# Performance work log

Hardware: AMD Instinct MI355X
Metric: run time of the kernel (lower is better)

## Reference

```python
import jax, jax.numpy as jnp
import numpy as np

B, T, N, F_IN, F_OUT, K = 4, 32, 1024, 128, 128, 4


def setup_inputs() -> dict:
    key = jax.random.key(0)
    k1, k2, k3 = jax.random.split(key, 3)
    X = jax.random.normal(k1, (B, T, N, F_IN), dtype=jnp.float32)
    # graph-shift operator; 1/sqrt(N) scaling keeps S^k products numerically tame
    S = jax.random.normal(k2, (N, N), dtype=jnp.float32) / np.float32(np.sqrt(N))
    W = jax.random.normal(k3, (F_OUT, F_IN, K), dtype=jnp.float32) * 0.1
    b = jnp.zeros((F_OUT,), dtype=jnp.float32)
    return {"X": X, "S": S, "W": W, "b": b}


def reference(X, S, W, b):
    # Y[:, t] = sum_{k=0}^{K-1, t-k>=0} S^k @ X[:, t-k] @ W[:, :, k]^T + b
    # (static graph: the per-(t,k) shift-chain product in the original collapses to S^k)
    Bsz, Tlen, Nn, Fin = X.shape
    Kord = W.shape[-1]
    Y = jnp.zeros((Bsz, Tlen, Nn, W.shape[0]), X.dtype)
    Z = X  # Z = S^k @ X, starting at k=0 (identity)
    for k in range(Kord):
        # causal time-shift by k: output at t uses Z at t-k (zeros for t-k<0)
        Zs = Z if k == 0 else jnp.pad(Z, ((0, 0), (k, 0), (0, 0), (0, 0)))[:, :Tlen]
        Y = Y + jnp.einsum('btnf,of->btno', Zs, W[:, :, k])
        if k < Kord - 1:
            Z = jnp.einsum('nm,btmf->btnf', S, Z)  # advance shift power
    return Y + b
```

## Files before the change

kernel.cpp:

```cpp
#include <hip/hip_runtime.h>
#include <stdint.h>

#define BT 128
#define NN 1024
#define FF 128

typedef __attribute__((ext_vector_type(8))) short short8;
typedef __attribute__((ext_vector_type(4))) float float4v;
typedef __attribute__((ext_vector_type(4))) unsigned short ushort4v;

__device__ __forceinline__ unsigned short f2bf(float f) {
  uint32_t u = __builtin_bit_cast(uint32_t, f);
  u += 0x7FFFu + ((u >> 16) & 1u);
  return (unsigned short)(u >> 16);
}

__device__ __forceinline__ void gload16(const void* g, void* l) {
  __builtin_amdgcn_global_load_lds(
      (const __attribute__((address_space(1))) uint32_t*)(g),
      (__attribute__((address_space(3))) uint32_t*)(l),
      16, 0, 0);
}

__global__ __launch_bounds__(256) void k_cvt_sw(const float* __restrict__ S,
                                                unsigned short* __restrict__ Sbf,
                                                unsigned short* __restrict__ SbfT,
                                                const float* __restrict__ W,
                                                unsigned short* __restrict__ Wk2) {
  __shared__ unsigned short tile[128 * 132];
  int tid = threadIdx.x;
  if (blockIdx.x >= 64) {
    int gid = (blockIdx.x - 64) * 256 + tid;
    int k = gid >> 14, o = (gid >> 7) & 127, f = gid & 127;
    Wk2[gid] = f2bf(W[(o * 128 + f) * 4 + k]);
    return;
  }
  int r0 = ((int)blockIdx.x >> 3) << 7;
  int c0 = ((int)blockIdx.x & 7) << 7;
#pragma unroll
  for (int i = 0; i < 16; ++i) {
    int idx = i * 256 + tid;
    int r = idx >> 5, cq = idx & 31;
    float4v v = reinterpret_cast<const float4v*>(S)[(size_t)(r0 + r) * 256 + (c0 >> 2) + cq];
    ushort4v h;
    h[0] = f2bf(v[0]); h[1] = f2bf(v[1]); h[2] = f2bf(v[2]); h[3] = f2bf(v[3]);
    *reinterpret_cast<ushort4v*>(&Sbf[(size_t)(r0 + r) * 1024 + c0 + cq * 4]) = h;
    *reinterpret_cast<ushort4v*>(&tile[r * 132 + cq * 4]) = h;
  }
  __syncthreads();
#pragma unroll
  for (int i = 0; i < 16; ++i) {
    int idx = i * 256 + tid;
    int c = idx >> 5, rq = idx & 31;
    ushort4v h;
#pragma unroll
    for (int j = 0; j < 4; ++j) h[j] = tile[(rq * 4 + j) * 132 + c];
    *reinterpret_cast<ushort4v*>(&SbfT[(size_t)(c0 + c) * 1024 + r0 + rq * 4]) = h;
  }
}

__global__ __launch_bounds__(256) void k_cvt_x(const float* __restrict__ X,
                                               unsigned short* __restrict__ Xbf,
                                               unsigned short* __restrict__ Xt) {
  __shared__ unsigned short tile[128 * 132];
  int bt = blockIdx.x >> 3;
  int n0 = (blockIdx.x & 7) << 7;
  int tid = threadIdx.x;
  size_t base = ((size_t)bt * NN + n0) * FF;
#pragma unroll
  for (int i = 0; i < 16; ++i) {
    int idx = i * 256 + tid;
    int e = idx * 4;
    int n = e >> 7, f = e & 127;
    float4v v = reinterpret_cast<const float4v*>(X + base)[idx];
    ushort4v h;
    h[0] = f2bf(v[0]); h[1] = f2bf(v[1]); h[2] = f2bf(v[2]); h[3] = f2bf(v[3]);
    reinterpret_cast<ushort4v*>(Xbf + base)[idx] = h;
    *reinterpret_cast<ushort4v*>(&tile[n * 132 + f]) = h;
  }
  __syncthreads();
  size_t tbase = (size_t)bt * (FF * NN);
#pragma unroll
  for (int i = 0; i < 64; ++i) {
    int idx = i * 256 + tid;
    int f = idx >> 7, n = idx & 127;
    Xt[tbase + (size_t)f * NN + n0 + n] = tile[n * 132 + f];
  }
}

__global__ __launch_bounds__(256) void gemm_s(const unsigned short* __restrict__ A,
                                              const unsigned short* __restrict__ B,
                                              unsigned short* __restrict__ C) {
  __shared__ unsigned short lA[128 * 64];
  __shared__ unsigned short lB[128 * 64];
  int r0 = ((int)blockIdx.x >> 3) << 7;
  int c0 = ((int)blockIdx.x & 7) << 7;
  int tid = threadIdx.x;
  int wave = tid >> 6, lane = tid & 63;
  int wr = wave >> 1, wc = wave & 1;
  int lr = lane & 15, g = lane >> 4;

  const unsigned short* gA = A + (size_t)r0 * 1024;
  const unsigned short* gB = B + (size_t)c0 * 1024;

  float4v acc[4][4];
#pragma unroll
  for (int a = 0; a < 4; ++a)
#pragma unroll
    for (int b = 0; b < 4; ++b) acc[a][b] = (float4v){0.f, 0.f, 0.f, 0.f};

  for (int kt = 0; kt < 16; ++kt) {
    int m0 = kt * 64;
#pragma unroll
    for (int i = 0; i < 4; ++i) {
      int id = i * 256 + tid;
      int row = id >> 3;
      int mc = (id & 7) << 3;
      int slot = (i * 256 + (tid & 192)) * 8;
      gload16(gA + (size_t)row * 1024 + m0 + mc, &lA[slot]);
      gload16(gB + (size_t)row * 1024 + m0 + mc, &lB[slot]);
    }
    __syncthreads();
#pragma unroll
    for (int kk = 0; kk < 2; ++kk) {
      short8 aF[4], bF[4];
#pragma unroll
      for (int mi = 0; mi < 4; ++mi)
        aF[mi] = *reinterpret_cast<const short8*>(
            &lA[(wr * 64 + mi * 16 + lr) * 64 + kk * 32 + g * 8]);
#pragma unroll
      for (int ni = 0; ni < 4; ++ni)
        bF[ni] = *reinterpret_cast<const short8*>(
            &lB[(wc * 64 + ni * 16 + lr) * 64 + kk * 32 + g * 8]);
#pragma unroll
      for (int mi = 0; mi < 4; ++mi)
#pragma unroll
        for (int ni = 0; ni < 4; ++ni)
          acc[mi][ni] = __builtin_amdgcn_mfma_f32_16x16x32_bf16(
              aF[mi], bF[ni], acc[mi][ni], 0, 0, 0);
    }
    __syncthreads();
  }

#pragma unroll
  for (int mi = 0; mi < 4; ++mi) {
#pragma unroll
    for (int ni = 0; ni < 4; ++ni) {
      int rr = r0 + wr * 64 + mi * 16 + g * 4;
      int cc = c0 + wc * 64 + ni * 16 + lr;
#pragma unroll
      for (int j = 0; j < 4; ++j)
        C[(size_t)(rr + j) * 1024 + cc] = f2bf(acc[mi][ni][j]);
    }
  }
}

__global__ __launch_bounds__(512, 2) void k_chain8(
    const unsigned short* __restrict__ Xt,
    const unsigned short* __restrict__ S1,
    const unsigned short* __restrict__ S2,
    const unsigned short* __restrict__ S3,
    unsigned short* __restrict__ Zn1,
    unsigned short* __restrict__ Zn2,
    unsigned short* __restrict__ Zn3) {
  extern __shared__ unsigned char lds[];

  int bid = blockIdx.x;
  int logical = (bid & 7) * 96 + (bid >> 3);
  int cblk = logical / 12;
  int pkn = logical - cblk * 12;
  int power = pkn >> 2, nblk = pkn & 3;
  const unsigned short* Sp = (power == 0) ? S1 : ((power == 1) ? S2 : S3);
  unsigned short* Zn = (power == 0) ? Zn1 : ((power == 1) ? Zn2 : Zn3);

  int tid = threadIdx.x;
  int wave = tid >> 6, lane = tid & 63;
  int wave_m = wave >> 2, wave_n = wave & 3;
  int lr = lane & 15, g = lane >> 4;

  unsigned srcO[4][2], dstO[4][2];
#pragma unroll
  for (int j = 0; j < 2; ++j) {
    int sr0 = wave * 16 + j * 8;
    int rbA = (sr0 & 63) + ((sr0 >> 6) << 7);
    int rbB = (sr0 & 31) + ((sr0 >> 5) << 6);
    int seg = lane & 7;
    int rA0 = rbA + (lane >> 3), rA1 = rA0 + 64;
    int rB0 = rbB + (lane >> 3), rB1 = rB0 + 32;
    srcO[0][j] = (unsigned)(cblk * 256 + rA0) * 1024u + (unsigned)((seg ^ (rA0 & 7)) << 3);
    srcO[3][j] = (unsigned)(cblk * 256 + rA1) * 1024u + (unsigned)((seg ^ (rA1 & 7)) << 3);
    srcO[1][j] = (unsigned)(nblk * 256 + rB0) * 1024u + (unsigned)((seg ^ (rB0 & 7)) << 3);
    srcO[2][j] = (unsigned)(nblk * 256 + rB1) * 1024u + (unsigned)((seg ^ (rB1 & 7)) << 3);
    dstO[0][j] = (unsigned)rbA * 128u;
    dstO[3][j] = (unsigned)(rbA + 64) * 128u;
    dstO[1][j] = 32768u + (unsigned)rbB * 128u;
    dstO[2][j] = 32768u + (unsigned)(rbB + 32) * 128u;
  }

  const unsigned xm = (unsigned)((lr & 7) << 4);
  const unsigned xo0 = ((unsigned)(g * 16)) ^ xm;
  const unsigned xo1 = ((unsigned)(64 + g * 16)) ^ xm;
  const unsigned aRB = (unsigned)((wave_m * 128 + lr) * 128);
  const unsigned bRB = 32768u + (unsigned)((wave_n * 64 + lr) * 128);

#define RD(OFF) (*reinterpret_cast<const short8*>(lds + (OFF)))

  float4v acc[8][4];
#pragma unroll
  for (int a = 0; a < 8; ++a)
#pragma unroll
    for (int b = 0; b < 4; ++b) acc[a][b] = (float4v){0.f, 0.f, 0.f, 0.f};

  short8 aF[4][2], bF[2][2], cF[2][2];

#pragma unroll
  for (int j = 0; j < 2; ++j) gload16(Xt + srcO[0][j], lds + dstO[0][j]);
#pragma unroll
  for (int j = 0; j < 2; ++j) gload16(Sp + srcO[1][j], lds + dstO[1][j]);
#pragma unroll
  for (int j = 0; j < 2; ++j) gload16(Sp + srcO[2][j], lds + dstO[2][j]);
#pragma unroll
  for (int j = 0; j < 2; ++j) gload16(Xt + srcO[3][j], lds + dstO[3][j]);
  asm volatile("s_waitcnt vmcnt(0)" ::: "memory");
  __builtin_amdgcn_s_barrier();

  for (int kt = 0; kt < 16; ++kt) {
    const unsigned bo = (unsigned)(kt & 1) << 16;
    const unsigned nbo = bo ^ 65536u;
    const unsigned ko = (unsigned)(kt + 1) * 64u;
    const bool st = (kt < 15);

#pragma unroll
    for (int mf = 0; mf < 4; ++mf) {
      aF[mf][0] = RD(bo + aRB + (unsigned)mf * 2048u + xo0);
      aF[mf][1] = RD(bo + aRB + (unsigned)mf * 2048u + xo1);
    }
#pragma unroll
    for (int nf = 0; nf < 2; ++nf) {
      bF[nf][0] = RD(bo + bRB + (unsigned)nf * 2048u + xo0);
      bF[nf][1] = RD(bo + bRB + (unsigned)nf * 2048u + xo1);
    }
    if (st) {
      gload16(Xt + srcO[0][0] + ko, lds + nbo + dstO[0][0]);
      gload16(Xt + srcO[0][1] + ko, lds + nbo + dstO[0][1]);
      asm volatile("s_waitcnt lgkmcnt(8) vmcnt(4)" ::: "memory");
    } else {
      asm volatile("s_waitcnt lgkmcnt(8) vmcnt(2)" ::: "memory");
    }
    __builtin_amdgcn_s_barrier();
    asm volatile("s_waitcnt lgkmcnt(0)" ::: "memory");
    __builtin_amdgcn_sched_barrier(0);
    __builtin_amdgcn_s_setprio(1);
#pragma unroll
    for (int mf = 0; mf < 4; ++mf)
#pragma unroll
      for (int nf = 0; nf < 2; ++nf) {
        acc[mf][nf] = __builtin_amdgcn_mfma_f32_16x16x32_bf16(aF[mf][0], bF[nf][0], acc[mf][nf], 0, 0, 0);
        acc[mf][nf] = __builtin_amdgcn_mfma_f32_16x16x32_bf16(aF[mf][1], bF[nf][1], acc[mf][nf], 0, 0, 0);
      }
    __builtin_amdgcn_s_setprio(0);
    __builtin_amdgcn_sched_barrier(0);
    __builtin_amdgcn_s_barrier();
    __builtin_amdgcn_sched_barrier(0);

#pragma unroll
    for (int nf = 0; nf < 2; ++nf) {
      cF[nf][0] = RD(bo + bRB + 4096u + (unsigned)nf * 2048u + xo0);
      cF[nf][1] = RD(bo + bRB + 4096u + (unsigned)nf * 2048u + xo1);
    }
    if (st) {
      gload16(Sp + srcO[1][0] + ko, lds + nbo + dstO[1][0]);
      gload16(Sp + srcO[1][1] + ko, lds + nbo + dstO[1][1]);
      asm volatile("s_waitcnt vmcnt(4)" ::: "memory");
    } else {
      asm volatile("s_waitcnt vmcnt(0)" ::: "memory");
    }
    __builtin_amdgcn_s_barrier();
    asm volatile("s_waitcnt lgkmcnt(0)" ::: "memory");
    __builtin_amdgcn_sched_barrier(0);
    __builtin_amdgcn_s_setprio(1);
#pragma unroll
    for (int mf = 0; mf < 4; ++mf)
#pragma unroll
      for (int nf = 0; nf < 2; ++nf) {
        acc[mf][2 + nf] = __builtin_amdgcn_mfma_f32_16x16x32_bf16(aF[mf][0], cF[nf][0], acc[mf][2 + nf], 0, 0, 0);
        acc[mf][2 + nf] = __builtin_amdgcn_mfma_f32_16x16x32_bf16(aF[mf][1], cF[nf][1], acc[mf][2 + nf], 0, 0, 0);
      }
    __builtin_amdgcn_s_setprio(0);
    __builtin_amdgcn_sched_barrier(0);
    __builtin_amdgcn_s_barrier();
    __builtin_amdgcn_sched_barrier(0);

#pragma unroll
    for (int mf = 0; mf < 4; ++mf) {
      aF[mf][0] = RD(bo + aRB + 8192u + (unsigned)mf * 2048u + xo0);
      aF[mf][1] = RD(bo + aRB + 8192u + (unsigned)mf * 2048u + xo1);
    }
    if (st) {
      gload16(Sp + srcO[2][0] + ko, lds + nbo + dstO[2][0]);
      gload16(Sp + srcO[2][1] + ko, lds + nbo + dstO[2][1]);
    }
    __builtin_amdgcn_s_barrier();
    asm volatile("s_waitcnt lgkmcnt(0)" ::: "memory");
    __builtin_amdgcn_sched_barrier(0);
    __builtin_amdgcn_s_setprio(1);
#pragma unroll
    for (int mf = 0; mf < 4; ++mf)
#pragma unroll
      for (int nf = 0; nf < 2; ++nf) {
        acc[4 + mf][nf] = __builtin_amdgcn_mfma_f32_16x16x32_bf16(aF[mf][0], bF[nf][0], acc[4 + mf][nf], 0, 0, 0);
        acc[4 + mf][nf] = __builtin_amdgcn_mfma_f32_16x16x32_bf16(aF[mf][1], bF[nf][1], acc[4 + mf][nf], 0, 0, 0);
      }
    __builtin_amdgcn_s_setprio(0);
    __builtin_amdgcn_sched_barrier(0);
    __builtin_amdgcn_s_barrier();
    __builtin_amdgcn_sched_barrier(0);

    if (st) {
      gload16(Xt + srcO[3][0] + ko, lds + nbo + dstO[3][0]);
      gload16(Xt + srcO[3][1] + ko, lds + nbo + dstO[3][1]);
      asm volatile("s_waitcnt vmcnt(4)" ::: "memory");
    }
    __builtin_amdgcn_s_barrier();
    __builtin_amdgcn_sched_barrier(0);
    __builtin_amdgcn_s_setprio(1);
#pragma unroll
    for (int mf = 0; mf < 4; ++mf)
#pragma unroll
      for (int nf = 0; nf < 2; ++nf) {
        acc[4 + mf][2 + nf] = __builtin_amdgcn_mfma_f32_16x16x32_bf16(aF[mf][0], cF[nf][0], acc[4 + mf][2 + nf], 0, 0, 0);
        acc[4 + mf][2 + nf] = __builtin_amdgcn_mfma_f32_16x16x32_bf16(aF[mf][1], cF[nf][1], acc[4 + mf][2 + nf], 0, 0, 0);
      }
    __builtin_amdgcn_s_setprio(0);
    __builtin_amdgcn_sched_barrier(0);
    __builtin_amdgcn_s_barrier();
    __builtin_amdgcn_sched_barrier(0);
  }
#undef RD

  int bt = cblk * 2 + wave_m;
  size_t zbase = (size_t)bt * (NN * FF);
  int nb = nblk * 256 + wave_n * 64 + lr;
#pragma unroll
  for (int i = 0; i < 8; ++i) {
#pragma unroll
    for (int j2 = 0; j2 < 4; ++j2) {
      int n = nb + j2 * 16;
      int f0 = i * 16 + g * 4;
      ushort4v pk;
#pragma unroll
      for (int j = 0; j < 4; ++j) pk[j] = f2bf(acc[i][j2][j]);
      *reinterpret_cast<ushort4v*>(&Zn[zbase + (size_t)n * FF + f0]) = pk;
    }
  }
}

__global__ __launch_bounds__(256) void k_out(const unsigned short* __restrict__ Xbf,
                                             const unsigned short* __restrict__ Zn1,
                                             const unsigned short* __restrict__ Zn2,
                                             const unsigned short* __restrict__ Zn3,
                                             const unsigned short* __restrict__ Wk2,
                                             const float* __restrict__ bias,
                                             float* __restrict__ Y) {
  __shared__ unsigned short lA[128 * 64];
  __shared__ unsigned short lB[128 * 64];
  int bid = blockIdx.x;
  int bt = bid >> 3;
  int n0 = (bid & 7) << 7;
  int t = bt & 31;
  int tid = threadIdx.x;
  int wave = tid >> 6, lane = tid & 63;
  int wr = wave >> 1, wc = wave & 1;
  int lr = lane & 15, g = lane >> 4;

  const unsigned short* Zs[4] = {Xbf, Zn1, Zn2, Zn3};

  float4v acc[4][4];
#pragma unroll
  for (int a = 0; a < 4; ++a)
#pragma unroll
    for (int b = 0; b < 4; ++b) acc[a][b] = (float4v){0.f, 0.f, 0.f, 0.f};

  for (int s = 0; s < 8; ++s) {
    int k = s >> 1;
    if (t < k) break;
    int fh = (s & 1) * 64;
    const unsigned short* gA = Zs[k] + ((size_t)(bt - k) * NN + n0) * FF;
    const unsigned short* gB = Wk2 + k * (FF * FF);
#pragma unroll
    for (int i = 0; i < 4; ++i) {
      int id = i * 256 + tid;
      int row = id >> 3;
      int fc = (id & 7) << 3;
      int slot = (i * 256 + (tid & 192)) * 8;
      gload16(gA + (size_t)row * FF + fh + fc, &lA[slot]);
      gload16(gB + (size_t)row * FF + fh + fc, &lB[slot]);
    }
    __syncthreads();
#pragma unroll
    for (int kk = 0; kk < 2; ++kk) {
      short8 aF[4], bF[4];
#pragma unroll
      for (int mi = 0; mi < 4; ++mi)
        aF[mi] = *reinterpret_cast<const short8*>(
            &lA[(wr * 64 + mi * 16 + lr) * 64 + kk * 32 + g * 8]);
#pragma unroll
      for (int ni = 0; ni < 4; ++ni)
        bF[ni] = *reinterpret_cast<const short8*>(
            &lB[(wc * 64 + ni * 16 + lr) * 64 + kk * 32 + g * 8]);
#pragma unroll
      for (int mi = 0; mi < 4; ++mi)
#pragma unroll
        for (int ni = 0; ni < 4; ++ni)
          acc[mi][ni] = __builtin_amdgcn_mfma_f32_16x16x32_bf16(
              aF[mi], bF[ni], acc[mi][ni], 0, 0, 0);
    }
    __syncthreads();
  }

  size_t obase = (size_t)bt * (NN * FF);
#pragma unroll
  for (int mi = 0; mi < 4; ++mi) {
#pragma unroll
    for (int ni = 0; ni < 4; ++ni) {
      int nloc = n0 + wr * 64 + mi * 16 + g * 4;
      int o = wc * 64 + ni * 16 + lr;
      float bv = bias[o];
#pragma unroll
      for (int j = 0; j < 4; ++j)
        Y[obase + (size_t)(nloc + j) * FF + o] = acc[mi][ni][j] + bv;
    }
  }
}


extern "C" void kernel_launch(void* const* d_in, const int* in_sizes, int n_in,
                              void* d_out, int out_size, void* d_ws, size_t ws_size,
                              hipStream_t stream) {
  const float* X = (const float*)d_in[0];
  const float* S = (const float*)d_in[1];
  const float* W = (const float*)d_in[2];
  const float* bvec = (const float*)d_in[3];
  float* Y = (float*)d_out;

  char* ws = (char*)d_ws;
  const size_t ZB = (size_t)BT * NN * FF * sizeof(unsigned short);
  const size_t SB = (size_t)1024 * 1024 * sizeof(unsigned short);
  unsigned short* Xt   = (unsigned short*)(ws + 0 * ZB);
  unsigned short* Zn1  = (unsigned short*)(ws + 1 * ZB);
  unsigned short* Zn2  = (unsigned short*)(ws + 2 * ZB);
  unsigned short* Zn3  = (unsigned short*)(ws + 3 * ZB);
  unsigned short* Xbf  = (unsigned short*)(ws + 4 * ZB);
  unsigned short* Sbf  = (unsigned short*)(ws + 5 * ZB);
  unsigned short* SbfT = (unsigned short*)(ws + 5 * ZB + 1 * SB);
  unsigned short* S2   = (unsigned short*)(ws + 5 * ZB + 2 * SB);
  unsigned short* S3   = (unsigned short*)(ws + 5 * ZB + 3 * SB);
  unsigned short* Wk2  = (unsigned short*)(ws + 5 * ZB + 4 * SB);

  k_cvt_sw<<<dim3(320), dim3(256), 0, stream>>>(S, Sbf, SbfT, W, Wk2);
  k_cvt_x<<<dim3(1024), dim3(256), 0, stream>>>(X, Xbf, Xt);

  gemm_s<<<dim3(64), dim3(256), 0, stream>>>(Sbf, SbfT, S2);
  gemm_s<<<dim3(64), dim3(256), 0, stream>>>(S2, SbfT, S3);

  hipError_t _e = hipFuncSetAttribute((const void*)k_chain8,
                      hipFuncAttributeMaxDynamicSharedMemorySize, 131072);
  (void)_e;
  k_chain8<<<dim3(768), dim3(512), 131072, stream>>>(Xt, Sbf, S2, S3, Zn1, Zn2, Zn3);

  k_out<<<dim3(1024), dim3(256), 0, stream>>>(Xbf, Zn1, Zn2, Zn3, Wk2, bvec, Y);
}
```

Baseline: 220.2 us.

## Restructure filter as Horner recurrence with fused time-shift and weight projection

Replaces the S^2/S^3 precompute, the three-power chain GEMM and the separate output GEMM with a Horner-style recurrence. It projects X by W3 first, then runs three S-multiply stages, each adding a fresh X·Wk projection in its epilogue, with the time shift done by reading the previous timestep (or a zero buffer). This drops the 1024^3 S-power GEMMs, the transposes and the 4-term output pass, cutting total work. In exchange it needs three dependent chain launches with only 256 blocks each, and error may compound through repeated bf16 rounding of the intermediates.

```diff
diff --git a/kernel.cpp b/kernel.cpp
--- a/kernel.cpp
+++ b/kernel.cpp
@@ -24,84 +24,59 @@
 
 __global__ __launch_bounds__(256) void k_cvt_sw(const float* __restrict__ S,
                                                 unsigned short* __restrict__ Sbf,
-                                                unsigned short* __restrict__ SbfT,
                                                 const float* __restrict__ W,
-                                                unsigned short* __restrict__ Wk2) {
-  __shared__ unsigned short tile[128 * 132];
+                                                unsigned short* __restrict__ Wk2,
+                                                unsigned short* __restrict__ zbuf) {
   int tid = threadIdx.x;
-  if (blockIdx.x >= 64) {
-    int gid = (blockIdx.x - 64) * 256 + tid;
+  int b = blockIdx.x;
+  if (b < 64) {
+#pragma unroll
+    for (int i = 0; i < 16; ++i) {
+      int g4 = b * 4096 + i * 256 + tid;
+      float4v v = reinterpret_cast<const float4v*>(S)[g4];
+      ushort4v h;
+      h[0] = f2bf(v[0]); h[1] = f2bf(v[1]); h[2] = f2bf(v[2]); h[3] = f2bf(v[3]);
+      reinterpret_cast<ushort4v*>(Sbf)[g4] = h;
+    }
+  } else if (b < 320) {
+    int gid = (b - 64) * 256 + tid;
     int k = gid >> 14, o = (gid >> 7) & 127, f = gid & 127;
     Wk2[gid] = f2bf(W[(o * 128 + f) * 4 + k]);
-    return;
-  }
-  int r0 = ((int)blockIdx.x >> 3) << 7;
-  int c0 = ((int)blockIdx.x & 7) << 7;
-#pragma unroll
-  for (int i = 0; i < 16; ++i) {
-    int idx = i * 256 + tid;
-    int r = idx >> 5, cq = idx & 31;
-    float4v v = reinterpret_cast<const float4v*>(S)[(size_t)(r0 + r) * 256 + (c0 >> 2) + cq];
+  } else {
+    ushort4v z = (ushort4v){0, 0, 0, 0};
+#pragma unroll
+    for (int i = 0; i < 16; ++i)
+      reinterpret_cast<ushort4v*>(zbuf)[(b - 320) * 4096 + i * 256 + tid] = z;
+  }
+}
+
+__global__ __launch_bounds__(256) void k_cvt_x(const float* __restrict__ X,
+                                               unsigned short* __restrict__ Xbf) {
+  int base = blockIdx.x * 1024 + threadIdx.x;
+#pragma unroll
+  for (int i = 0; i < 4; ++i) {
+    int g4 = base + i * 256;
+    float4v v = reinterpret_cast<const float4v*>(X)[g4];
     ushort4v h;
     h[0] = f2bf(v[0]); h[1] = f2bf(v[1]); h[2] = f2bf(v[2]); h[3] = f2bf(v[3]);
-    *reinterpret_cast<ushort4v*>(&Sbf[(size_t)(r0 + r) * 1024 + c0 + cq * 4]) = h;
-    *reinterpret_cast<ushort4v*>(&tile[r * 132 + cq * 4]) = h;
-  }
-  __syncthreads();
-#pragma unroll
-  for (int i = 0; i < 16; ++i) {
-    int idx = i * 256 + tid;
-    int c = idx >> 5, rq = idx & 31;
-    ushort4v h;
-#pragma unroll
-    for (int j = 0; j < 4; ++j) h[j] = tile[(rq * 4 + j) * 132 + c];
-    *reinterpret_cast<ushort4v*>(&SbfT[(size_t)(c0 + c) * 1024 + r0 + rq * 4]) = h;
-  }
-}
-
-__global__ __launch_bounds__(256) void k_cvt_x(const float* __restrict__ X,
-                                               unsigned short* __restrict__ Xbf,
-                                               unsigned short* __restrict__ Xt) {
-  __shared__ unsigned short tile[128 * 132];
+    reinterpret_cast<ushort4v*>(Xbf)[g4] = h;
+  }
+}
+
+__global__ __launch_bounds__(256) void k_proj(const unsigned short* __restrict__ Wk2,
+                                              const unsigned short* __restrict__ Xbf,
+                                              unsigned short* __restrict__ U3) {
+  __shared__ unsigned short lA[128 * 64];
+  __shared__ unsigned short lB[128 * 64];
   int bt = blockIdx.x >> 3;
   int n0 = (blockIdx.x & 7) << 7;
-  int tid = threadIdx.x;
-  size_t base = ((size_t)bt * NN + n0) * FF;
-#pragma unroll
-  for (int i = 0; i < 16; ++i) {
-    int idx = i * 256 + tid;
-    int e = idx * 4;
-    int n = e >> 7, f = e & 127;
-    float4v v = reinterpret_cast<const float4v*>(X + base)[idx];
-    ushort4v h;
-    h[0] = f2bf(v[0]); h[1] = f2bf(v[1]); h[2] = f2bf(v[2]); h[3] = f2bf(v[3]);
-    reinterpret_cast<ushort4v*>(Xbf + base)[idx] = h;
-    *reinterpret_cast<ushort4v*>(&tile[n * 132 + f]) = h;
-  }
-  __syncthreads();
-  size_t tbase = (size_t)bt * (FF * NN);
-#pragma unroll
-  for (int i = 0; i < 64; ++i) {
-    int idx = i * 256 + tid;
-    int f = idx >> 7, n = idx & 127;
-    Xt[tbase + (size_t)f * NN + n0 + n] = tile[n * 132 + f];
-  }
-}
-
-__global__ __launch_bounds__(256) void gemm_s(const unsigned short* __restrict__ A,
-                                              const unsigned short* __restrict__ B,
-                                              unsigned short* __restrict__ C) {
-  __shared__ unsigned short lA[128 * 64];
-  __shared__ unsigned short lB[128 * 64];
-  int r0 = ((int)blockIdx.x >> 3) << 7;
-  int c0 = ((int)blockIdx.x & 7) << 7;
   int tid = threadIdx.x;
   int wave = tid >> 6, lane = tid & 63;
   int wr = wave >> 1, wc = wave & 1;
   int lr = lane & 15, g = lane >> 4;
 
-  const unsigned short* gA = A + (size_t)r0 * 1024;
-  const unsigned short* gB = B + (size_t)c0 * 1024;
+  const unsigned short* gA = Wk2 + 3 * (FF * FF);
+  const unsigned short* gB = Xbf + (size_t)bt * (NN * FF) + (size_t)n0 * FF;
 
   float4v acc[4][4];
 #pragma unroll
@@ -109,7 +84,7 @@
 #pragma unroll
     for (int b = 0; b < 4; ++b) acc[a][b] = (float4v){0.f, 0.f, 0.f, 0.f};
 
-  for (int kt = 0; kt < 16; ++kt) {
+  for (int kt = 0; kt < 2; ++kt) {
     int m0 = kt * 64;
 #pragma unroll
     for (int i = 0; i < 4; ++i) {
@@ -117,8 +92,8 @@
       int row = id >> 3;
       int mc = (id & 7) << 3;
       int slot = (i * 256 + (tid & 192)) * 8;
-      gload16(gA + (size_t)row * 1024 + m0 + mc, &lA[slot]);
-      gload16(gB + (size_t)row * 1024 + m0 + mc, &lB[slot]);
+      gload16(gA + (size_t)row * 128 + m0 + mc, &lA[slot]);
+      gload16(gB + (size_t)row * 128 + m0 + mc, &lB[slot]);
     }
     __syncthreads();
 #pragma unroll
@@ -142,43 +117,49 @@
     __syncthreads();
   }
 
+  unsigned short* Uo = U3 + (size_t)bt * (NN * FF);
 #pragma unroll
   for (int mi = 0; mi < 4; ++mi) {
 #pragma unroll
     for (int ni = 0; ni < 4; ++ni) {
-      int rr = r0 + wr * 64 + mi * 16 + g * 4;
-      int cc = c0 + wc * 64 + ni * 16 + lr;
+      int o = wr * 64 + mi * 16 + g * 4;
+      int n = n0 + wc * 64 + ni * 16 + lr;
 #pragma unroll
       for (int j = 0; j < 4; ++j)
-        C[(size_t)(rr + j) * 1024 + cc] = f2bf(acc[mi][ni][j]);
-    }
-  }
-}
-
-__global__ __launch_bounds__(512, 2) void k_chain8(
-    const unsigned short* __restrict__ Xt,
-    const unsigned short* __restrict__ S1,
-    const unsigned short* __restrict__ S2,
-    const unsigned short* __restrict__ S3,
-    unsigned short* __restrict__ Zn1,
-    unsigned short* __restrict__ Zn2,
-    unsigned short* __restrict__ Zn3) {
+        Uo[(size_t)(o + j) * NN + n] = f2bf(acc[mi][ni][j]);
+    }
+  }
+}
+
+template <bool FINAL>
+__global__ __launch_bounds__(512, 2) void k_chain(
+    const unsigned short* __restrict__ Uin,
+    const unsigned short* __restrict__ Sbf,
+    const unsigned short* __restrict__ Wg,
+    const unsigned short* __restrict__ Xbf,
+    const unsigned short* __restrict__ zbuf,
+    unsigned short* __restrict__ Hout,
+    float* __restrict__ Yout,
+    const float* __restrict__ bias) {
   extern __shared__ unsigned char lds[];
 
   int bid = blockIdx.x;
-  int logical = (bid & 7) * 96 + (bid >> 3);
-  int cblk = logical / 12;
-  int pkn = logical - cblk * 12;
-  int power = pkn >> 2, nblk = pkn & 3;
-  const unsigned short* Sp = (power == 0) ? S1 : ((power == 1) ? S2 : S3);
-  unsigned short* Zn = (power == 0) ? Zn1 : ((power == 1) ? Zn2 : Zn3);
+  int logical = (bid & 7) * 32 + (bid >> 3);
+  int cblk = logical >> 2;
+  int nblk = logical & 3;
 
   int tid = threadIdx.x;
   int wave = tid >> 6, lane = tid & 63;
   int wave_m = wave >> 2, wave_n = wave & 3;
   int lr = lane & 15, g = lane >> 4;
 
-  unsigned srcO[4][2], dstO[4][2];
+  const int bt0 = cblk * 2;
+  const bool t0z = ((bt0 & 31) == 0);
+  const unsigned short* A0 = t0z ? zbuf : (Uin + (size_t)(bt0 - 1) * (NN * FF));
+  const unsigned short* A1 = Uin + (size_t)bt0 * (NN * FF);
+
+  const unsigned short* pS[4][2];
+  unsigned dstO[4][2];
 #pragma unroll
   for (int j = 0; j < 2; ++j) {
     int sr0 = wave * 16 + j * 8;
@@ -187,10 +168,12 @@
     int seg = lane & 7;
     int rA0 = rbA + (lane >> 3), rA1 = rA0 + 64;
     int rB0 = rbB + (lane >> 3), rB1 = rB0 + 32;
-    srcO[0][j] = (unsigned)(cblk * 256 + rA0) * 1024u + (unsigned)((seg ^ (rA0 & 7)) << 3);
-    srcO[3][j] = (unsigned)(cblk * 256 + rA1) * 1024u + (unsigned)((seg ^ (rA1 & 7)) << 3);
-    srcO[1][j] = (unsigned)(nblk * 256 + rB0) * 1024u + (unsigned)((seg ^ (rB0 & 7)) << 3);
-    srcO[2][j] = (unsigned)(nblk * 256 + rB1) * 1024u + (unsigned)((seg ^ (rB1 & 7)) << 3);
+    pS[0][j] = (rA0 < 128 ? A0 + (size_t)rA0 * NN : A1 + (size_t)(rA0 - 128) * NN)
+               + ((seg ^ (rA0 & 7)) << 3);
+    pS[3][j] = (rA1 < 128 ? A0 + (size_t)rA1 * NN : A1 + (size_t)(rA1 - 128) * NN)
+               + ((seg ^ (rA1 & 7)) << 3);
+    pS[1][j] = Sbf + (size_t)(nblk * 256 + rB0) * NN + ((seg ^ (rB0 & 7)) << 3);
+    pS[2][j] = Sbf + (size_t)(nblk * 256 + rB1) * NN + ((seg ^ (rB1 & 7)) << 3);
     dstO[0][j] = (unsigned)rbA * 128u;
     dstO[3][j] = (unsigned)(rbA + 64) * 128u;
     dstO[1][j] = 32768u + (unsigned)rbB * 128u;
@@ -214,13 +197,9 @@
   short8 aF[4][2], bF[2][2], cF[2][2];
 
 #pragma unroll
-  for (int j = 0; j < 2; ++j) gload16(Xt + srcO[0][j], lds + dstO[0][j]);
-#pragma unroll
-  for (int j = 0; j < 2; ++j) gload16(Sp + srcO[1][j], lds + dstO[1][j]);
-#pragma unroll
-  for (int j = 0; j < 2; ++j) gload16(Sp + srcO[2][j], lds + dstO[2][j]);
-#pragma unroll
-  for (int j = 0; j < 2; ++j) gload16(Xt + srcO[3][j], lds + dstO[3][j]);
+  for (int s = 0; s < 4; ++s)
+#pragma unroll
+    for (int j = 0; j < 2; ++j) gload16(pS[s][j], lds + dstO[s][j]);
   asm volatile("s_waitcnt vmcnt(0)" ::: "memory");
   __builtin_amdgcn_s_barrier();
 
@@ -241,8 +220,8 @@
       bF[nf][1] = RD(bo + bRB + (unsigned)nf * 2048u + xo1);
     }
     if (st) {
-      gload16(Xt + srcO[0][0] + ko, lds + nbo + dstO[0][0]);
-      gload16(Xt + srcO[0][1] + ko, lds + nbo + dstO[0][1]);
+      gload16(pS[0][0] + ko, lds + nbo + dstO[0][0]);
+      gload16(pS[0][1] + ko, lds + nbo + dstO[0][1]);
       asm volatile("s_waitcnt lgkmcnt(8) vmcnt(4)" ::: "memory");
     } else {
       asm volatile("s_waitcnt lgkmcnt(8) vmcnt(2)" ::: "memory");
@@ -269,8 +248,8 @@
       cF[nf][1] = RD(bo + bRB + 4096u + (unsigned)nf * 2048u + xo1);
     }
     if (st) {
-      gload16(Sp + srcO[1][0] + ko, lds + nbo + dstO[1][0]);
-      gload16(Sp + srcO[1][1] + ko, lds + nbo + dstO[1][1]);
+      gload16(pS[1][0] + ko, lds + nbo + dstO[1][0]);
+      gload16(pS[1][1] + ko, lds + nbo + dstO[1][1]);
       asm volatile("s_waitcnt vmcnt(4)" ::: "memory");
     } else {
       asm volatile("s_waitcnt vmcnt(0)" ::: "memory");
@@ -297,8 +276,8 @@
       aF[mf][1] = RD(bo + aRB + 8192u + (unsigned)mf * 2048u + xo1);
     }
     if (st) {
-      gload16(Sp + srcO[2][0] + ko, lds + nbo + dstO[2][0]);
-      gload16(Sp + srcO[2][1] + ko, lds + nbo + dstO[2][1]);
+      gload16(pS[2][0] + ko, lds + nbo + dstO[2][0]);
+      gload16(pS[2][1] + ko, lds + nbo + dstO[2][1]);
     }
     __builtin_amdgcn_s_barrier();
     asm volatile("s_waitcnt lgkmcnt(0)" ::: "memory");
@@ -317,8 +296,8 @@
     __builtin_amdgcn_sched_barrier(0);
 
     if (st) {
-      gload16(Xt + srcO[3][0] + ko, lds + nbo + dstO[3][0]);
-      gload16(Xt + srcO[3][1] + ko, lds + nbo + dstO[3][1]);
+      gload16(pS[3][0] + ko, lds + nbo + dstO[3][0]);
+      gload16(pS[3][1] + ko, lds + nbo + dstO[3][1]);
       asm volatile("s_waitcnt vmcnt(4)" ::: "memory");
     }
     __builtin_amdgcn_s_barrier();
@@ -338,97 +317,51 @@
   }
 #undef RD
 
-  int bt = cblk * 2 + wave_m;
-  size_t zbase = (size_t)bt * (NN * FF);
-  int nb = nblk * 256 + wave_n * 64 + lr;
-#pragma unroll
-  for (int i = 0; i < 8; ++i) {
-#pragma unroll
-    for (int j2 = 0; j2 < 4; ++j2) {
-      int n = nb + j2 * 16;
-      int f0 = i * 16 + g * 4;
-      ushort4v pk;
-#pragma unroll
-      for (int j = 0; j < 4; ++j) pk[j] = f2bf(acc[i][j2][j]);
-      *reinterpret_cast<ushort4v*>(&Zn[zbase + (size_t)n * FF + f0]) = pk;
-    }
-  }
-}
-
-__global__ __launch_bounds__(256) void k_out(const unsigned short* __restrict__ Xbf,
-                                             const unsigned short* __restrict__ Zn1,
-                                             const unsigned short* __restrict__ Zn2,
-                                             const unsigned short* __restrict__ Zn3,
-                                             const unsigned short* __restrict__ Wk2,
-                                             const float* __restrict__ bias,
-                                             float* __restrict__ Y) {
-  __shared__ unsigned short lA[128 * 64];
-  __shared__ unsigned short lB[128 * 64];
-  int bid = blockIdx.x;
-  int bt = bid >> 3;
-  int n0 = (bid & 7) << 7;
-  int t = bt & 31;
-  int tid = threadIdx.x;
-  int wave = tid >> 6, lane = tid & 63;
-  int wr = wave >> 1, wc = wave & 1;
-  int lr = lane & 15, g = lane >> 4;
-
-  const unsigned short* Zs[4] = {Xbf, Zn1, Zn2, Zn3};
-
-  float4v acc[4][4];
-#pragma unroll
-  for (int a = 0; a < 4; ++a)
-#pragma unroll
-    for (int b = 0; b < 4; ++b) acc[a][b] = (float4v){0.f, 0.f, 0.f, 0.f};
-
-  for (int s = 0; s < 8; ++s) {
-    int k = s >> 1;
-    if (t < k) break;
-    int fh = (s & 1) * 64;
-    const unsigned short* gA = Zs[k] + ((size_t)(bt - k) * NN + n0) * FF;
-    const unsigned short* gB = Wk2 + k * (FF * FF);
-#pragma unroll
-    for (int i = 0; i < 4; ++i) {
-      int id = i * 256 + tid;
-      int row = id >> 3;
-      int fc = (id & 7) << 3;
-      int slot = (i * 256 + (tid & 192)) * 8;
-      gload16(gA + (size_t)row * FF + fh + fc, &lA[slot]);
-      gload16(gB + (size_t)row * FF + fh + fc, &lB[slot]);
-    }
-    __syncthreads();
-#pragma unroll
-    for (int kk = 0; kk < 2; ++kk) {
-      short8 aF[4], bF[4];
-#pragma unroll
-      for (int mi = 0; mi < 4; ++mi)
-        aF[mi] = *reinterpret_cast<const short8*>(
-            &lA[(wr * 64 + mi * 16 + lr) * 64 + kk * 32 + g * 8]);
-#pragma unroll
-      for (int ni = 0; ni < 4; ++ni)
-        bF[ni] = *reinterpret_cast<const short8*>(
-            &lB[(wc * 64 + ni * 16 + lr) * 64 + kk * 32 + g * 8]);
-#pragma unroll
-      for (int mi = 0; mi < 4; ++mi)
-#pragma unroll
-        for (int ni = 0; ni < 4; ++ni)
-          acc[mi][ni] = __builtin_amdgcn_mfma_f32_16x16x32_bf16(
-              aF[mi], bF[ni], acc[mi][ni], 0, 0, 0);
-    }
-    __syncthreads();
-  }
-
-  size_t obase = (size_t)bt * (NN * FF);
-#pragma unroll
-  for (int mi = 0; mi < 4; ++mi) {
-#pragma unroll
-    for (int ni = 0; ni < 4; ++ni) {
-      int nloc = n0 + wr * 64 + mi * 16 + g * 4;
-      int o = wc * 64 + ni * 16 + lr;
-      float bv = bias[o];
-#pragma unroll
-      for (int j = 0; j < 4; ++j)
-        Y[obase + (size_t)(nloc + j) * FF + o] = acc[mi][ni][j] + bv;
+  int bt = bt0 + wave_m;
+  const unsigned short* Xb = Xbf + (size_t)bt * (NN * FF);
+  const int nbase = nblk * 256 + wave_n * 64;
+#pragma unroll 1
+  for (int kk = 0; kk < 4; ++kk) {
+    int fc = kk * 32 + g * 8;
+    short8 aW[8], bW[4];
+#pragma unroll
+    for (int mf = 0; mf < 8; ++mf)
+      aW[mf] = *reinterpret_cast<const short8*>(Wg + (size_t)(mf * 16 + lr) * FF + fc);
+#pragma unroll
+    for (int nf = 0; nf < 4; ++nf)
+      bW[nf] = *reinterpret_cast<const short8*>(Xb + (size_t)(nbase + nf * 16 + lr) * FF + fc);
+#pragma unroll
+    for (int mf = 0; mf < 8; ++mf)
+#pragma unroll
+      for (int nf = 0; nf < 4; ++nf)
+        acc[mf][nf] = __builtin_amdgcn_mfma_f32_16x16x32_bf16(aW[mf], bW[nf], acc[mf][nf], 0, 0, 0);
+  }
+
+  if constexpr (FINAL) {
+    float* Yp = Yout + (size_t)bt * (NN * FF);
+#pragma unroll
+    for (int i = 0; i < 8; ++i) {
+      int o0 = i * 16 + g * 4;
+      float4v bv = *reinterpret_cast<const float4v*>(bias + o0);
+#pragma unroll
+      for (int j2 = 0; j2 < 4; ++j2) {
+        int n = nbase + j2 * 16 + lr;
+        float4v r = acc[i][j2] + bv;
+        *reinterpret_cast<float4v*>(Yp + (size_t)n * FF + o0) = r;
+      }
+    }
+  } else {
+    unsigned short* Hp = Hout + (size_t)bt * (NN * FF);
+#pragma unroll
+    for (int i = 0; i < 8; ++i) {
+      int o0 = i * 16 + g * 4;
+#pragma unroll
+      for (int j2 = 0; j2 < 4; ++j2) {
+        int n = nbase + j2 * 16 + lr;
+#pragma unroll
+        for (int j = 0; j < 4; ++j)
+          Hp[(size_t)(o0 + j) * NN + n] = f2bf(acc[i][j2][j]);
+      }
     }
   }
 }
@@ -445,28 +378,28 @@
 
   char* ws = (char*)d_ws;
   const size_t ZB = (size_t)BT * NN * FF * sizeof(unsigned short);
-  const size_t SB = (size_t)1024 * 1024 * sizeof(unsigned short);
-  unsigned short* Xt   = (unsigned short*)(ws + 0 * ZB);
-  unsigned short* Zn1  = (unsigned short*)(ws + 1 * ZB);
-  unsigned short* Zn2  = (unsigned short*)(ws + 2 * ZB);
-  unsigned short* Zn3  = (unsigned short*)(ws + 3 * ZB);
-  unsigned short* Xbf  = (unsigned short*)(ws + 4 * ZB);
-  unsigned short* Sbf  = (unsigned short*)(ws + 5 * ZB);
-  unsigned short* SbfT = (unsigned short*)(ws + 5 * ZB + 1 * SB);
-  unsigned short* S2   = (unsigned short*)(ws + 5 * ZB + 2 * SB);
-  unsigned short* S3   = (unsigned short*)(ws + 5 * ZB + 3 * SB);
-  unsigned short* Wk2  = (unsigned short*)(ws + 5 * ZB + 4 * SB);
-
-  k_cvt_sw<<<dim3(320), dim3(256), 0, stream>>>(S, Sbf, SbfT, W, Wk2);
-  k_cvt_x<<<dim3(1024), dim3(256), 0, stream>>>(X, Xbf, Xt);
-
-  gemm_s<<<dim3(64), dim3(256), 0, stream>>>(Sbf, SbfT, S2);
-  gemm_s<<<dim3(64), dim3(256), 0, stream>>>(S2, SbfT, S3);
-
-  hipError_t _e = hipFuncSetAttribute((const void*)k_chain8,
+  unsigned short* Xbf = (unsigned short*)(ws + 0 * ZB);
+  unsigned short* U3  = (unsigned short*)(ws + 1 * ZB);
+  unsigned short* H2  = (unsigned short*)(ws + 2 * ZB);
+  unsigned short* H1  = (unsigned short*)(ws + 3 * ZB);
+  unsigned short* Sbf = (unsigned short*)(ws + 4 * ZB);
+  unsigned short* Wk2 = (unsigned short*)(ws + 4 * ZB + (size_t)2097152);
+  unsigned short* zbf = (unsigned short*)(ws + 4 * ZB + (size_t)2097152 + 131072);
+
+  k_cvt_sw<<<dim3(328), dim3(256), 0, stream>>>(S, Sbf, W, Wk2, zbf);
+  k_cvt_x<<<dim3(4096), dim3(256), 0, stream>>>(X, Xbf);
+  k_proj<<<dim3(1024), dim3(256), 0, stream>>>(Wk2, Xbf, U3);
+
+  hipError_t e0 = hipFuncSetAttribute((const void*)k_chain<false>,
                       hipFuncAttributeMaxDynamicSharedMemorySize, 131072);
-  (void)_e;
-  k_chain8<<<dim3(768), dim3(512), 131072, stream>>>(Xt, Sbf, S2, S3, Zn1, Zn2, Zn3);
-
-  k_out<<<dim3(1024), dim3(256), 0, stream>>>(Xbf, Zn1, Zn2, Zn3, Wk2, bvec, Y);
-}
+  hipError_t e1 = hipFuncSetAttribute((const void*)k_chain<true>,
+                      hipFuncAttributeMaxDynamicSharedMemorySize, 131072);
+  (void)e0; (void)e1;
+
+  k_chain<false><<<dim3(256), dim3(512), 131072, stream>>>(
+      U3, Sbf, Wk2 + 2 * (FF * FF), Xbf, zbf, H2, nullptr, nullptr);
+  k_chain<false><<<dim3(256), dim3(512), 131072, stream>>>(
+      H2, Sbf, Wk2 + 1 * (FF * FF), Xbf, zbf, H1, nullptr, nullptr);
+  k_chain<true><<<dim3(256), dim3(512), 131072, stream>>>(
+      H1, Sbf, Wk2, Xbf, zbf, nullptr, Y, bvec);
+}
```

New measurement: 178.2 us. 19.1% less time.
